# Kernel tuning notes

Hardware: AMD Instinct MI355X
Metric: run time of the kernel (lower is better)

The kernel has to match this reference:

```python
import jax, jax.numpy as jnp
import numpy as np

B, T, S, E = 16, 1024, 1024, 1024  # note: module requires T == E (see bmm shape constraint)


def setup_inputs() -> dict:
    key = jax.random.key(0)
    ks = jax.random.split(key, 11)
    w = lambda k: jax.random.normal(k, (E, E), dtype=jnp.float32) * 0.02
    b = lambda k: jax.random.normal(k, (E,), dtype=jnp.float32) * 0.02
    return {
        "query": jax.random.normal(ks[0], (B, T, E), dtype=jnp.float32),
        "key": jax.random.normal(ks[1], (B, S, E), dtype=jnp.float32),
        "value": jax.random.normal(ks[2], (B, S, E), dtype=jnp.float32),
        "Wq": w(ks[3]), "bq": b(ks[4]),
        "Wk": w(ks[5]), "bk": b(ks[6]),
        "Wv": w(ks[7]), "bv": b(ks[8]),
        "Wo": w(ks[9]), "bo": b(ks[10]),
    }


def reference(query, key, value, Wq, bq, Wk, bk, Wv, bv, Wo, bo):
    # torch Linear: y = x @ W.T + b
    q = query @ Wq.T + bq          # [B, T, E]
    k = key @ Wk.T + bk            # [B, S, E]
    v = value @ Wv.T + bv          # [B, S, E]
    # Faithful to source: BOTH q and k are transposed to [B, E, len] before bmm,
    # so weights[b, i, s] = sum_t q[b, t, i] * k[b, s, t]  (requires T == E).
    scale = 1.0 / jnp.sqrt(jnp.asarray(q.shape[-1], q.dtype))
    w = jnp.einsum('bti,bst->bis', q, k) * scale   # [B, E, S]
    a = jax.nn.softmax(w, axis=-1)                 # softmax over src_len
    o = jnp.einsum('bis,bse->bie', a, v)           # [B, E, E]
    return o @ Wo.T + bo
```

## Files before the change

### kernel.cpp

```cpp
#include <hip/hip_runtime.h>
#include <hip/hip_bf16.h>
#include <stdint.h>

typedef __attribute__((ext_vector_type(8))) short short8;
typedef __attribute__((ext_vector_type(4))) float floatx4;

#define MODE_PROJ_T 0
#define MODE_PROJ_N 1
#define MODE_SCORES 2
#define MODE_ATT    3
#define MODE_OUT    4

__device__ __forceinline__ unsigned short f2bf(float f) {
    union { float f; unsigned int u; } x; x.f = f;
    unsigned int u = x.u + 0x7FFFu + ((x.u >> 16) & 1u);
    return (unsigned short)(u >> 16);
}

__device__ __forceinline__ void gload_lds16(const void* g, void* lds) {
    __builtin_amdgcn_global_load_lds(
        (const __attribute__((address_space(1))) unsigned int*)g,
        (__attribute__((address_space(3))) unsigned int*)lds,
        16, 0, 0);
}

template<int MODE>
__device__ __forceinline__ void gemm_body(
    const __hip_bfloat16* __restrict__ A,
    const __hip_bfloat16* __restrict__ Bm,
    const float* __restrict__ bias,
    void* __restrict__ Cout,
    int K, long sA, long sB, long sC, float alpha,
    int id, short* As, short* Bs)
{
    const int tid  = threadIdx.x;
    const int wid  = tid >> 6;
    const int lane = tid & 63;

    const int xcd = id & 7;
    const int s   = id >> 3;
    int bx, by, bz;
    if (MODE == MODE_SCORES || MODE == MODE_ATT) {
        bz = xcd + ((s >> 6) << 3);
        by = (s >> 3) & 7;
        bx = s & 7;
    } else {
        bz = 0;
        bx = s >> 4;
        by = ((s & 15) << 3) | xcd;
    }
    const int row0 = by * 128;
    const int col0 = bx * 128;

    const __hip_bfloat16* Ab = A  + (size_t)bz * sA;
    const __hip_bfloat16* Bb = Bm + (size_t)bz * sB;

    floatx4 acc[4][4];
#pragma unroll
    for (int i = 0; i < 4; i++)
#pragma unroll
        for (int j = 0; j < 4; j++) acc[i][j] = (floatx4){0.f, 0.f, 0.f, 0.f};

    const int l7   = lane & 7;
    const int l3   = lane >> 3;
    const int cblk = ((l7 ^ l3) << 3);
    const int wm   = wid >> 1, wn = wid & 1;
    const int l15  = lane & 15, quad = lane >> 4;

    for (int k0 = 0; k0 < K; k0 += 64) {
        __syncthreads();
#pragma unroll
        for (int i = 0; i < 4; i++) {
            const int c = wid * 4 + i;
            const int r = c * 8 + l3;
            gload_lds16(Ab + (size_t)(row0 + r) * 1024 + k0 + cblk, As + c * 512);
            gload_lds16(Bb + (size_t)(col0 + r) * 1024 + k0 + cblk, Bs + c * 512);
        }
        __syncthreads();
#pragma unroll
        for (int ks = 0; ks < 2; ks++) {
            short8 af[4], bfr[4];
            const int kb = (((ks * 4 + quad) ^ l7) << 3);
#pragma unroll
            for (int t = 0; t < 4; t++) {
                af[t]  = *(const short8*)&As[(wm * 64 + t * 16 + l15) * 64 + kb];
                bfr[t] = *(const short8*)&Bs[(wn * 64 + t * 16 + l15) * 64 + kb];
            }
#pragma unroll
            for (int mt = 0; mt < 4; mt++)
#pragma unroll
                for (int nt = 0; nt < 4; nt++)
                    acc[mt][nt] = __builtin_amdgcn_mfma_f32_16x16x32_bf16(
                        af[mt], bfr[nt], acc[mt][nt], 0, 0, 0);
        }
    }

#pragma unroll
    for (int nt = 0; nt < 4; nt++) {
        const int col = col0 + wn * 64 + nt * 16 + l15;
        float bv = 0.f;
        if (MODE == MODE_PROJ_T || MODE == MODE_PROJ_N || MODE == MODE_OUT) bv = bias[col];
#pragma unroll
        for (int mt = 0; mt < 4; mt++) {
            const int rbase = row0 + wm * 64 + mt * 16 + quad * 4;
#pragma unroll
            for (int r = 0; r < 4; r++) {
                const int m = rbase + r;
                float v = acc[mt][nt][r];
                if (MODE == MODE_SCORES) v *= alpha;
                v += bv;
                if (MODE == MODE_SCORES) {
                    ((float*)Cout)[(size_t)bz * sC + (size_t)m * 1024 + col] = v;
                } else if (MODE == MODE_OUT) {
                    ((float*)Cout)[(size_t)m * 1024 + col] = v;
                } else if (MODE == MODE_PROJ_N || MODE == MODE_ATT) {
                    ((unsigned short*)Cout)[(size_t)bz * sC + (size_t)m * 1024 + col] = f2bf(v);
                } else {
                    ((unsigned short*)Cout)[((size_t)(m >> 10) << 20) + (size_t)col * 1024 + (m & 1023)] = f2bf(v);
                }
            }
        }
    }
}

template<int MODE>
__global__ __launch_bounds__(256) void gemm_nt(
    const __hip_bfloat16* __restrict__ A,
    const __hip_bfloat16* __restrict__ Bm,
    const float* __restrict__ bias,
    void* __restrict__ Cout,
    int K, long sA, long sB, long sC, float alpha)
{
    __shared__ short As[128 * 64];
    __shared__ short Bs[128 * 64];
    gemm_body<MODE>(A, Bm, bias, Cout, K, sA, sB, sC, alpha, blockIdx.x, As, Bs);
}

__global__ __launch_bounds__(256) void gemm_proj3(
    const __hip_bfloat16* __restrict__ qb, const __hip_bfloat16* __restrict__ kb,
    const __hip_bfloat16* __restrict__ vb,
    const __hip_bfloat16* __restrict__ wq, const __hip_bfloat16* __restrict__ wk,
    const __hip_bfloat16* __restrict__ wv,
    const float* __restrict__ biq, const float* __restrict__ bik,
    const float* __restrict__ biv,
    unsigned short* __restrict__ qT, unsigned short* __restrict__ kp,
    unsigned short* __restrict__ vT)
{
    __shared__ short As[128 * 64];
    __shared__ short Bs[128 * 64];
    const int id  = blockIdx.x;
    const int g   = id >> 10;
    const int lid = id & 1023;
    const __hip_bfloat16* A;  const __hip_bfloat16* B;  const float* bias;  void* C;
    if      (g == 0) { A = qb; B = wq; bias = biq; C = qT; }
    else if (g == 1) { A = kb; B = wk; bias = bik; C = kp; }
    else             { A = vb; B = wv; bias = biv; C = vT; }
    if (g == 1) gemm_body<MODE_PROJ_N>(A, B, bias, C, 1024, 0, 0, 0, 1.f, lid, As, Bs);
    else        gemm_body<MODE_PROJ_T>(A, B, bias, C, 1024, 0, 0, 0, 1.f, lid, As, Bs);
}

__global__ __launch_bounds__(256) void softmax_rows(
    const float* __restrict__ S, unsigned short* __restrict__ A)
{
    const int row  = blockIdx.x * 4 + (threadIdx.x >> 6);
    const int lane = threadIdx.x & 63;
    const float4* p = (const float4*)(S + (size_t)row * 1024);
    float4 v[4];
    float mx = -3.0e38f;
#pragma unroll
    for (int i = 0; i < 4; i++) {
        v[i] = p[lane + i * 64];
        mx = fmaxf(mx, fmaxf(fmaxf(v[i].x, v[i].y), fmaxf(v[i].z, v[i].w)));
    }
#pragma unroll
    for (int off = 32; off >= 1; off >>= 1) mx = fmaxf(mx, __shfl_xor(mx, off, 64));
    float e[16], sum = 0.f;
#pragma unroll
    for (int i = 0; i < 4; i++) {
        e[i*4+0] = __expf(v[i].x - mx); e[i*4+1] = __expf(v[i].y - mx);
        e[i*4+2] = __expf(v[i].z - mx); e[i*4+3] = __expf(v[i].w - mx);
        sum += e[i*4+0] + e[i*4+1] + e[i*4+2] + e[i*4+3];
    }
#pragma unroll
    for (int off = 32; off >= 1; off >>= 1) sum += __shfl_xor(sum, off, 64);
    const float inv = 1.0f / sum;
    ushort4* out = (ushort4*)(A + (size_t)row * 1024);
#pragma unroll
    for (int i = 0; i < 4; i++) {
        ushort4 o;
        o.x = f2bf(e[i*4+0] * inv); o.y = f2bf(e[i*4+1] * inv);
        o.z = f2bf(e[i*4+2] * inv); o.w = f2bf(e[i*4+3] * inv);
        out[lane + i * 64] = o;
    }
}

__global__ __launch_bounds__(256) void cvt_all(
    const float* __restrict__ q, const float* __restrict__ k, const float* __restrict__ v,
    const float* __restrict__ wq, const float* __restrict__ wk,
    const float* __restrict__ wv, const float* __restrict__ wo,
    unsigned short* __restrict__ qb, unsigned short* __restrict__ kb, unsigned short* __restrict__ vb,
    unsigned short* __restrict__ wqb, unsigned short* __restrict__ wkb,
    unsigned short* __restrict__ wvb, unsigned short* __restrict__ wob)
{
    const int id = blockIdx.x;
    const float* src; unsigned short* dst; int base;
    if      (id < 16384) { src = q;  dst = qb;  base = 0; }
    else if (id < 32768) { src = k;  dst = kb;  base = 16384; }
    else if (id < 49152) { src = v;  dst = vb;  base = 32768; }
    else if (id < 50176) { src = wq; dst = wqb; base = 49152; }
    else if (id < 51200) { src = wk; dst = wkb; base = 50176; }
    else if (id < 52224) { src = wv; dst = wvb; base = 51200; }
    else                 { src = wo; dst = wob; base = 52224; }
    const int i = (id - base) * 256 + threadIdx.x;
    const float4 vv = ((const float4*)src)[i];
    ushort4 o; o.x = f2bf(vv.x); o.y = f2bf(vv.y); o.z = f2bf(vv.z); o.w = f2bf(vv.w);
    ((ushort4*)dst)[i] = o;
}

extern "C" void kernel_launch(void* const* d_in, const int* in_sizes, int n_in,
                              void* d_out, int out_size, void* d_ws, size_t ws_size,
                              hipStream_t stream) {
    const float* query = (const float*)d_in[0];
    const float* key   = (const float*)d_in[1];
    const float* value = (const float*)d_in[2];
    const float* Wq = (const float*)d_in[3];  const float* bq = (const float*)d_in[4];
    const float* Wk = (const float*)d_in[5];  const float* bk = (const float*)d_in[6];
    const float* Wv = (const float*)d_in[7];  const float* bv = (const float*)d_in[8];
    const float* Wo = (const float*)d_in[9];  const float* bo = (const float*)d_in[10];

    char* ws = (char*)d_ws;
    const size_t MB = 1ull << 20;
    unsigned short* qbf = (unsigned short*)(ws + 0   * MB);
    unsigned short* kbf = (unsigned short*)(ws + 32  * MB);
    unsigned short* vbf = (unsigned short*)(ws + 64  * MB);
    unsigned short* wqb = (unsigned short*)(ws + 96  * MB);
    unsigned short* wkb = (unsigned short*)(ws + 98  * MB);
    unsigned short* wvb = (unsigned short*)(ws + 100 * MB);
    unsigned short* wob = (unsigned short*)(ws + 102 * MB);
    unsigned short* qT  = (unsigned short*)(ws + 104 * MB);
    unsigned short* kp  = (unsigned short*)(ws + 136 * MB);
    unsigned short* vT  = (unsigned short*)(ws + 168 * MB);
    float*          sc  = (float*)(ws + 0 * MB);
    unsigned short* att = (unsigned short*)(ws + 64 * MB);
    unsigned short* ob  = (unsigned short*)(ws + 104 * MB);

    const long S1M = 1 << 20;
    dim3 blk(256);

    cvt_all<<<53248, blk, 0, stream>>>(query, key, value, Wq, Wk, Wv, Wo,
                                       qbf, kbf, vbf, wqb, wkb, wvb, wob);

    gemm_proj3<<<3072, blk, 0, stream>>>(
        (const __hip_bfloat16*)qbf, (const __hip_bfloat16*)kbf, (const __hip_bfloat16*)vbf,
        (const __hip_bfloat16*)wqb, (const __hip_bfloat16*)wkb, (const __hip_bfloat16*)wvb,
        bq, bk, bv, qT, kp, vT);

    gemm_nt<MODE_SCORES><<<1024, blk, 0, stream>>>(
        (const __hip_bfloat16*)qT, (const __hip_bfloat16*)kp, nullptr, sc, 1024,
        S1M, S1M, S1M, 0.03125f);

    softmax_rows<<<4096, blk, 0, stream>>>(sc, att);

    gemm_nt<MODE_ATT><<<1024, blk, 0, stream>>>(
        (const __hip_bfloat16*)att, (const __hip_bfloat16*)vT, nullptr, ob, 1024,
        S1M, S1M, S1M, 1.f);

    gemm_nt<MODE_OUT><<<1024, blk, 0, stream>>>(
        (const __hip_bfloat16*)ob, (const __hip_bfloat16*)wob, bo, d_out, 1024, 0, 0, 0, 1.f);
}
```

Measured before the change: 540.8 us.

## Replace GEMM core with 256x256 8-wave double-buffered pipelined kernel

Replaces the 128x128 single-buffered 4-wave GEMM body with a 256x256 tile computed by 8 waves. The new body double-buffers LDS and issues async global-to-LDS loads for the next k-tiles in half-tile chunks interleaved with four MFMA phases, using explicit vmcnt waits, barriers and setprio. The aim is to hide memory latency and raise operand reuse per loaded byte. In exchange it uses 128KB of LDS per block and many more accumulator registers. Grids shrink four-fold, which may leave CUs underfilled on the 256-block launches.

```diff
diff --git a/kernel.cpp b/kernel.cpp
--- a/kernel.cpp
+++ b/kernel.cpp
@@ -24,75 +24,161 @@
         16, 0, 0);
 }
 
+
+__device__ __forceinline__ void stage_half_A(
+    const __hip_bfloat16* __restrict__ Ab, short* lds,
+    int row0, int k0, int h, int wid, int lane)
+{
+    const int rl = lane >> 3, sl = lane & 7;
+    const int gcol = k0 + ((sl ^ rl) << 3);
+#pragma unroll
+    for (int j = 0; j < 2; j++) {
+        const int c = wid * 2 + j;
+        const int lrow = ((c >> 3) << 7) + h * 64 + ((c & 7) << 3);
+        gload_lds16(Ab + (size_t)(row0 + lrow + rl) * 1024 + gcol, lds + lrow * 64);
+    }
+}
+
+__device__ __forceinline__ void stage_half_B(
+    const __hip_bfloat16* __restrict__ Bb, short* lds,
+    int col0, int k0, int h, int wid, int lane)
+{
+    const int rl = lane >> 3, sl = lane & 7;
+    const int gcol = k0 + ((sl ^ rl) << 3);
+#pragma unroll
+    for (int j = 0; j < 2; j++) {
+        const int c = wid * 2 + j;
+        const int lrow = ((c >> 2) << 6) + h * 32 + ((c & 3) << 3);
+        gload_lds16(Bb + (size_t)(col0 + lrow + rl) * 1024 + gcol, lds + lrow * 64);
+    }
+}
+
 template<int MODE>
-__device__ __forceinline__ void gemm_body(
+__device__ __forceinline__ void gemm_body8(
     const __hip_bfloat16* __restrict__ A,
     const __hip_bfloat16* __restrict__ Bm,
     const float* __restrict__ bias,
     void* __restrict__ Cout,
     int K, long sA, long sB, long sC, float alpha,
-    int id, short* As, short* Bs)
+    int row0, int col0, int bz, short* As0, short* Bs0)
 {
     const int tid  = threadIdx.x;
     const int wid  = tid >> 6;
     const int lane = tid & 63;
-
-    const int xcd = id & 7;
-    const int s   = id >> 3;
-    int bx, by, bz;
-    if (MODE == MODE_SCORES || MODE == MODE_ATT) {
-        bz = xcd + ((s >> 6) << 3);
-        by = (s >> 3) & 7;
-        bx = s & 7;
-    } else {
-        bz = 0;
-        bx = s >> 4;
-        by = ((s & 15) << 3) | xcd;
-    }
-    const int row0 = by * 128;
-    const int col0 = bx * 128;
+    const int wm = wid >> 2, wn = wid & 3;
+    const int l15 = lane & 15, quad = lane >> 4, l7 = lane & 7;
 
     const __hip_bfloat16* Ab = A  + (size_t)bz * sA;
     const __hip_bfloat16* Bb = Bm + (size_t)bz * sB;
-
-    floatx4 acc[4][4];
-#pragma unroll
-    for (int i = 0; i < 4; i++)
+    const int NT = K >> 6;
+
+    floatx4 acc[8][4];
+#pragma unroll
+    for (int i = 0; i < 8; i++)
 #pragma unroll
         for (int j = 0; j < 4; j++) acc[i][j] = (floatx4){0.f, 0.f, 0.f, 0.f};
 
-    const int l7   = lane & 7;
-    const int l3   = lane >> 3;
-    const int cblk = ((l7 ^ l3) << 3);
-    const int wm   = wid >> 1, wn = wid & 1;
-    const int l15  = lane & 15, quad = lane >> 4;
-
-    for (int k0 = 0; k0 < K; k0 += 64) {
-        __syncthreads();
-#pragma unroll
-        for (int i = 0; i < 4; i++) {
-            const int c = wid * 4 + i;
-            const int r = c * 8 + l3;
-            gload_lds16(Ab + (size_t)(row0 + r) * 1024 + k0 + cblk, As + c * 512);
-            gload_lds16(Bb + (size_t)(col0 + r) * 1024 + k0 + cblk, Bs + c * 512);
-        }
-        __syncthreads();
-#pragma unroll
-        for (int ks = 0; ks < 2; ks++) {
-            short8 af[4], bfr[4];
-            const int kb = (((ks * 4 + quad) ^ l7) << 3);
-#pragma unroll
-            for (int t = 0; t < 4; t++) {
-                af[t]  = *(const short8*)&As[(wm * 64 + t * 16 + l15) * 64 + kb];
-                bfr[t] = *(const short8*)&Bs[(wn * 64 + t * 16 + l15) * 64 + kb];
-            }
+    stage_half_B(Bb, Bs0, col0, 0, 0, wid, lane);
+    stage_half_A(Ab, As0, row0, 0, 0, wid, lane);
+    stage_half_B(Bb, Bs0, col0, 0, 1, wid, lane);
+    stage_half_A(Ab, As0, row0, 0, 1, wid, lane);
+    asm volatile("s_waitcnt vmcnt(4)" ::: "memory");
+    stage_half_A(Ab, As0 + 16384, row0, 64, 0, wid, lane);
+    stage_half_B(Bb, Bs0 + 16384, col0, 64, 1, wid, lane);
+    stage_half_A(Ab, As0 + 16384, row0, 64, 1, wid, lane);
+    asm volatile("s_waitcnt vmcnt(6)" ::: "memory");
+    __builtin_amdgcn_s_barrier();
+
+    for (int t = 0; t < NT; ++t) {
+        const int d = t & 1;
+        short* Asd = As0 + d * 16384;
+        short* Bsd = Bs0 + d * 16384;
+        short* Asn = As0 + (d ^ 1) * 16384;
+        short* Bsn = Bs0 + (d ^ 1) * 16384;
+        const int k1 = (t + 1) << 6, k2 = (t + 2) << 6;
+        short8 af[4][2], bfr[4][2];
+
+#pragma unroll
+        for (int mt = 0; mt < 4; mt++)
+#pragma unroll
+            for (int ks = 0; ks < 2; ks++)
+                af[mt][ks] = *(const short8*)&Asd[(wm * 128 + mt * 16 + l15) * 64 +
+                                                  ((((ks << 2) + quad) ^ l7) << 3)];
+#pragma unroll
+        for (int nt = 0; nt < 2; nt++)
+#pragma unroll
+            for (int ks = 0; ks < 2; ks++)
+                bfr[nt][ks] = *(const short8*)&Bsd[(wn * 64 + nt * 16 + l15) * 64 +
+                                                   ((((ks << 2) + quad) ^ l7) << 3)];
+        if (t + 1 < NT) stage_half_B(Bb, Bsn, col0, k1, 0, wid, lane);
+        __builtin_amdgcn_s_barrier();
+        __builtin_amdgcn_s_setprio(1);
+#pragma unroll
+        for (int ks = 0; ks < 2; ks++)
 #pragma unroll
             for (int mt = 0; mt < 4; mt++)
 #pragma unroll
-                for (int nt = 0; nt < 4; nt++)
+                for (int nt = 0; nt < 2; nt++)
                     acc[mt][nt] = __builtin_amdgcn_mfma_f32_16x16x32_bf16(
-                        af[mt], bfr[nt], acc[mt][nt], 0, 0, 0);
-        }
+                        af[mt][ks], bfr[nt][ks], acc[mt][nt], 0, 0, 0);
+        __builtin_amdgcn_s_setprio(0);
+        __builtin_amdgcn_s_barrier();
+
+#pragma unroll
+        for (int nt = 0; nt < 2; nt++)
+#pragma unroll
+            for (int ks = 0; ks < 2; ks++)
+                bfr[2 + nt][ks] = *(const short8*)&Bsd[(wn * 64 + (2 + nt) * 16 + l15) * 64 +
+                                                       ((((ks << 2) + quad) ^ l7) << 3)];
+        if (t + 2 < NT) stage_half_A(Ab, Asd, row0, k2, 0, wid, lane);
+        __builtin_amdgcn_s_barrier();
+        __builtin_amdgcn_s_setprio(1);
+#pragma unroll
+        for (int ks = 0; ks < 2; ks++)
+#pragma unroll
+            for (int mt = 0; mt < 4; mt++)
+#pragma unroll
+                for (int nt = 0; nt < 2; nt++)
+                    acc[mt][2 + nt] = __builtin_amdgcn_mfma_f32_16x16x32_bf16(
+                        af[mt][ks], bfr[2 + nt][ks], acc[mt][2 + nt], 0, 0, 0);
+        __builtin_amdgcn_s_setprio(0);
+        __builtin_amdgcn_s_barrier();
+
+#pragma unroll
+        for (int mt = 0; mt < 4; mt++)
+#pragma unroll
+            for (int ks = 0; ks < 2; ks++)
+                af[mt][ks] = *(const short8*)&Asd[(wm * 128 + (4 + mt) * 16 + l15) * 64 +
+                                                  ((((ks << 2) + quad) ^ l7) << 3)];
+        if (t + 2 < NT) stage_half_B(Bb, Bsd, col0, k2, 1, wid, lane);
+        __builtin_amdgcn_s_barrier();
+        __builtin_amdgcn_s_setprio(1);
+#pragma unroll
+        for (int ks = 0; ks < 2; ks++)
+#pragma unroll
+            for (int mt = 0; mt < 4; mt++)
+#pragma unroll
+                for (int nt = 0; nt < 2; nt++)
+                    acc[4 + mt][2 + nt] = __builtin_amdgcn_mfma_f32_16x16x32_bf16(
+                        af[mt][ks], bfr[2 + nt][ks], acc[4 + mt][2 + nt], 0, 0, 0);
+        __builtin_amdgcn_s_setprio(0);
+        __builtin_amdgcn_s_barrier();
+
+        if (t + 2 < NT) stage_half_A(Ab, Asd, row0, k2, 1, wid, lane);
+        __builtin_amdgcn_s_barrier();
+        __builtin_amdgcn_s_setprio(1);
+#pragma unroll
+        for (int ks = 0; ks < 2; ks++)
+#pragma unroll
+            for (int mt = 0; mt < 4; mt++)
+#pragma unroll
+                for (int nt = 0; nt < 2; nt++)
+                    acc[4 + mt][nt] = __builtin_amdgcn_mfma_f32_16x16x32_bf16(
+                        af[mt][ks], bfr[nt][ks], acc[4 + mt][nt], 0, 0, 0);
+        __builtin_amdgcn_s_setprio(0);
+        if (t + 2 < NT) asm volatile("s_waitcnt vmcnt(6)" ::: "memory");
+        else            asm volatile("s_waitcnt vmcnt(0)" ::: "memory");
+        __builtin_amdgcn_s_barrier();
     }
 
 #pragma unroll
@@ -101,8 +187,8 @@
         float bv = 0.f;
         if (MODE == MODE_PROJ_T || MODE == MODE_PROJ_N || MODE == MODE_OUT) bv = bias[col];
 #pragma unroll
-        for (int mt = 0; mt < 4; mt++) {
-            const int rbase = row0 + wm * 64 + mt * 16 + quad * 4;
+        for (int mt = 0; mt < 8; mt++) {
+            const int rbase = row0 + wm * 128 + mt * 16 + quad * 4;
 #pragma unroll
             for (int r = 0; r < 4; r++) {
                 const int m = rbase + r;
@@ -124,19 +210,33 @@
 }
 
 template<int MODE>
-__global__ __launch_bounds__(256) void gemm_nt(
+__global__ __launch_bounds__(512, 2) void gemm8(
     const __hip_bfloat16* __restrict__ A,
     const __hip_bfloat16* __restrict__ Bm,
     const float* __restrict__ bias,
     void* __restrict__ Cout,
     int K, long sA, long sB, long sC, float alpha)
 {
-    __shared__ short As[128 * 64];
-    __shared__ short Bs[128 * 64];
-    gemm_body<MODE>(A, Bm, bias, Cout, K, sA, sB, sC, alpha, blockIdx.x, As, Bs);
-}
-
-__global__ __launch_bounds__(256) void gemm_proj3(
+    __shared__ __align__(16) short As[2 * 256 * 64];
+    __shared__ __align__(16) short Bs[2 * 256 * 64];
+    const int id = blockIdx.x;
+    const int xcd = id & 7;
+    const int s   = id >> 3;
+    int by, bx, bz;
+    if (MODE == MODE_SCORES || MODE == MODE_ATT) {
+        bz = xcd + ((s >> 4) << 3);
+        by = (s & 15) >> 2;
+        bx = s & 3;
+    } else {
+        bz = 0;
+        by = ((s >> 2) << 3) | xcd;
+        bx = s & 3;
+    }
+    gemm_body8<MODE>(A, Bm, bias, Cout, K, sA, sB, sC, alpha,
+                     by * 256, bx * 256, bz, As, Bs);
+}
+
+__global__ __launch_bounds__(512, 2) void gemm8_proj3(
     const __hip_bfloat16* __restrict__ qb, const __hip_bfloat16* __restrict__ kb,
     const __hip_bfloat16* __restrict__ vb,
     const __hip_bfloat16* __restrict__ wq, const __hip_bfloat16* __restrict__ wk,
@@ -146,17 +246,23 @@
     unsigned short* __restrict__ qT, unsigned short* __restrict__ kp,
     unsigned short* __restrict__ vT)
 {
-    __shared__ short As[128 * 64];
-    __shared__ short Bs[128 * 64];
+    __shared__ __align__(16) short As[2 * 256 * 64];
+    __shared__ __align__(16) short Bs[2 * 256 * 64];
     const int id  = blockIdx.x;
-    const int g   = id >> 10;
-    const int lid = id & 1023;
+    const int xcd = id & 7;
+    const int s   = id >> 3;
+    const int g   = s >> 5;
+    const int s2  = s & 31;
+    const int by  = ((s2 >> 2) << 3) | xcd;
+    const int bx  = s2 & 3;
     const __hip_bfloat16* A;  const __hip_bfloat16* B;  const float* bias;  void* C;
     if      (g == 0) { A = qb; B = wq; bias = biq; C = qT; }
     else if (g == 1) { A = kb; B = wk; bias = bik; C = kp; }
     else             { A = vb; B = wv; bias = biv; C = vT; }
-    if (g == 1) gemm_body<MODE_PROJ_N>(A, B, bias, C, 1024, 0, 0, 0, 1.f, lid, As, Bs);
-    else        gemm_body<MODE_PROJ_T>(A, B, bias, C, 1024, 0, 0, 0, 1.f, lid, As, Bs);
+    if (g == 1) gemm_body8<MODE_PROJ_N>(A, B, bias, C, 1024, 0, 0, 0, 1.f,
+                                        by * 256, bx * 256, 0, As, Bs);
+    else        gemm_body8<MODE_PROJ_T>(A, B, bias, C, 1024, 0, 0, 0, 1.f,
+                                        by * 256, bx * 256, 0, As, Bs);
 }
 
 __global__ __launch_bounds__(256) void softmax_rows(
@@ -246,25 +352,26 @@
 
     const long S1M = 1 << 20;
     dim3 blk(256);
+    dim3 blk5(512);
 
     cvt_all<<<53248, blk, 0, stream>>>(query, key, value, Wq, Wk, Wv, Wo,
                                        qbf, kbf, vbf, wqb, wkb, wvb, wob);
 
-    gemm_proj3<<<3072, blk, 0, stream>>>(
+    gemm8_proj3<<<768, blk5, 0, stream>>>(
         (const __hip_bfloat16*)qbf, (const __hip_bfloat16*)kbf, (const __hip_bfloat16*)vbf,
         (const __hip_bfloat16*)wqb, (const __hip_bfloat16*)wkb, (const __hip_bfloat16*)wvb,
         bq, bk, bv, qT, kp, vT);
 
-    gemm_nt<MODE_SCORES><<<1024, blk, 0, stream>>>(
+    gemm8<MODE_SCORES><<<256, blk5, 0, stream>>>(
         (const __hip_bfloat16*)qT, (const __hip_bfloat16*)kp, nullptr, sc, 1024,
         S1M, S1M, S1M, 0.03125f);
 
     softmax_rows<<<4096, blk, 0, stream>>>(sc, att);
 
-    gemm_nt<MODE_ATT><<<1024, blk, 0, stream>>>(
+    gemm8<MODE_ATT><<<256, blk5, 0, stream>>>(
         (const __hip_bfloat16*)att, (const __hip_bfloat16*)vT, nullptr, ob, 1024,
         S1M, S1M, S1M, 1.f);
 
-    gemm_nt<MODE_OUT><<<1024, blk, 0, stream>>>(
+    gemm8<MODE_OUT><<<256, blk5, 0, stream>>>(
         (const __hip_bfloat16*)ob, (const __hip_bfloat16*)wob, bo, d_out, 1024, 0, 0, 0, 1.f);
 }
```

New measurement: 537.7 us. Within noise of the previous version (-0.6%).
